# Optimization experiments

Hardware: AMD Instinct MI355X
Metric: run time of the kernel (lower is better)

Reference implementation:

```python
import jax, jax.numpy as jnp
import numpy as np

N, T, D, H = 32, 1024, 1152, 16
DH = D // H            # 72
MLP = int(D * 4.0)     # 4608
EPS = 1e-6


def setup_inputs() -> dict:
    key = jax.random.key(0)
    ks = jax.random.split(key, 14)
    s = 0.02
    return {
        "x": jax.random.normal(ks[0], (N, T, D), jnp.float32),
        "c": jax.random.normal(ks[1], (N, D), jnp.float32),
        "qkv_w": jax.random.normal(ks[2], (D, 3 * D), jnp.float32) * s,
        "qkv_b": jax.random.normal(ks[3], (3 * D,), jnp.float32) * s,
        "proj_w": jax.random.normal(ks[4], (D, D), jnp.float32) * s,
        "proj_b": jax.random.normal(ks[5], (D,), jnp.float32) * s,
        "fc1_w": jax.random.normal(ks[6], (D, MLP), jnp.float32) * s,
        "fc1_b": jax.random.normal(ks[7], (MLP,), jnp.float32) * s,
        "fc2_w": jax.random.normal(ks[8], (MLP, D), jnp.float32) * s,
        "fc2_b": jax.random.normal(ks[9], (D,), jnp.float32) * s,
        "ada_w": jax.random.normal(ks[10], (D, 6 * D), jnp.float32) * s,
        "ada_b": jax.random.normal(ks[11], (6 * D,), jnp.float32) * s,
    }


def _layernorm(x):
    m = jnp.mean(x, axis=-1, keepdims=True)
    v = jnp.var(x, axis=-1, keepdims=True)
    return (x - m) * jax.lax.rsqrt(v + EPS)


def _modulate(x, shift, scale):
    # shift, scale: (N, D) broadcast over T
    return x * (1.0 + scale[:, None, :]) + shift[:, None, :]


def _attention(x, qkv_w, qkv_b, proj_w, proj_b):
    n, t, d = x.shape
    scale = DH ** (-0.5)
    qkv = x @ qkv_w + qkv_b                       # (N,T,3D)
    qkv = qkv.reshape(n, t, 3, H, DH)
    q, k, v = qkv[:, :, 0], qkv[:, :, 1], qkv[:, :, 2]  # each (N,T,H,DH)
    # Faithful to source: matmul over the LAST two dims -> per-token
    # head-vs-head attention of shape (N,T,H,H), softmax over heads.
    attn = jnp.einsum("nthd,ntkd->nthk", q * scale, k)
    attn = jax.nn.softmax(attn, axis=-1)
    out = jnp.einsum("nthk,ntkd->nthd", attn, v)  # (N,T,H,DH)
    out = out.transpose(0, 2, 1, 3).reshape(n, t, d)  # faithful scramble
    return out @ proj_w + proj_b


def _mlp(x, fc1_w, fc1_b, fc2_w, fc2_b):
    h = jax.nn.gelu(x @ fc1_w + fc1_b, approximate=False)  # exact GELU (torch default)
    return h @ fc2_w + fc2_b


def reference(x, c, qkv_w, qkv_b, proj_w, proj_b, fc1_w, fc1_b, fc2_w, fc2_b,
              ada_w, ada_b):
    ada = jax.nn.silu(c) @ ada_w + ada_b          # (N, 6D)
    (shift_msa, scale_msa, gate_msa,
     shift_mlp, scale_mlp, gate_mlp) = jnp.split(ada, 6, axis=1)
    x = x + gate_msa[:, None, :] * _attention(
        _modulate(_layernorm(x), shift_msa, scale_msa),
        qkv_w, qkv_b, proj_w, proj_b)
    x = x + gate_mlp[:, None, :] * _mlp(
        _modulate(_layernorm(x), shift_mlp, scale_mlp),
        fc1_w, fc1_b, fc2_w, fc2_b)
    return x
```

## Files before the change

kernel.cpp:

```cpp
#include <hip/hip_runtime.h>

#define DEV __device__ __forceinline__

typedef __attribute__((ext_vector_type(8))) short short8;
typedef __attribute__((ext_vector_type(8))) __bf16 bf16x8;
typedef __attribute__((ext_vector_type(4))) float f32x4;

#define TD      1024
#define DD      1152
#define DHH     72
#define MLPD    4608
#define QKVN    3456
#define ADAN    6912
#define MROWS   32768

DEV unsigned short f32_to_bf16(float f) {
  unsigned int u = __float_as_uint(f);
  u += 0x7fffu + ((u >> 16) & 1u);
  return (unsigned short)(u >> 16);
}

DEV void gl16(const void* g, void* l) {
  __builtin_amdgcn_global_load_lds((__attribute__((address_space(1))) void*)g,
                                   (__attribute__((address_space(3))) void*)l,
                                   16, 0, 0);
}

DEV bf16x8 zero_bf16x8() {
  short8 z = {0, 0, 0, 0, 0, 0, 0, 0};
  return __builtin_bit_cast(bf16x8, z);
}

DEV float gelu_exact(float v) {
  return 0.5f * v * (1.0f + erff(v * 0.70710678118654752f));
}

#define WAITV(n) asm volatile("s_waitcnt vmcnt(" #n ")" ::: "memory")

__global__ __launch_bounds__(256) void wtrans_kernel(const float* __restrict__ W,
                                                     unsigned short* __restrict__ Wt,
                                                     int K, int N) {
  __shared__ unsigned short tile[32][33];
  const int nb = blockIdx.x * 32, kb = blockIdx.y * 32;
  const int tx = threadIdx.x, ty = threadIdx.y;
  #pragma unroll
  for (int i = ty; i < 32; i += 8)
    tile[i][tx] = f32_to_bf16(W[(size_t)(kb + i) * N + nb + tx]);
  __syncthreads();
  #pragma unroll
  for (int i = ty; i < 32; i += 8)
    Wt[(size_t)(nb + i) * K + kb + tx] = tile[tx][i];
}

__global__ __launch_bounds__(256) void ada_kernel(const float* __restrict__ c,
                                                  const float* __restrict__ ada_w,
                                                  const float* __restrict__ ada_b,
                                                  float* __restrict__ ada_out) {
  __shared__ float sc[DD];
  const int n = blockIdx.y;
  const int col = blockIdx.x * 256 + threadIdx.x;
  for (int i = threadIdx.x; i < DD; i += 256) {
    float v = c[(size_t)n * DD + i];
    sc[i] = v / (1.0f + __expf(-v));
  }
  __syncthreads();
  float acc = ada_b[col];
  #pragma unroll 8
  for (int k = 0; k < DD; ++k)
    acc += sc[k] * ada_w[(size_t)k * ADAN + col];
  ada_out[(size_t)n * ADAN + col] = acc;
}

__global__ __launch_bounds__(256) void ln_mod_kernel(const float* __restrict__ X,
                                                     const float* __restrict__ ada,
                                                     int soff,
                                                     unsigned short* __restrict__ out) {
  const int row = blockIdx.x;
  const int batch = row >> 10;
  const float* xr = X + (size_t)row * DD;
  const int t = threadIdx.x;

  float4 v0 = reinterpret_cast<const float4*>(xr)[t];
  float4 v1 = make_float4(0.f, 0.f, 0.f, 0.f);
  const bool has2 = (t < 32);
  if (has2) v1 = reinterpret_cast<const float4*>(xr)[256 + t];

  float s  = v0.x + v0.y + v0.z + v0.w + v1.x + v1.y + v1.z + v1.w;
  float sq = v0.x*v0.x + v0.y*v0.y + v0.z*v0.z + v0.w*v0.w
           + v1.x*v1.x + v1.y*v1.y + v1.z*v1.z + v1.w*v1.w;
  #pragma unroll
  for (int m = 1; m < 64; m <<= 1) {
    s  += __shfl_xor(s, m);
    sq += __shfl_xor(sq, m);
  }
  __shared__ float red[8];
  const int wv = t >> 6;
  if ((t & 63) == 0) { red[wv] = s; red[4 + wv] = sq; }
  __syncthreads();
  s  = red[0] + red[1] + red[2] + red[3];
  sq = red[4] + red[5] + red[6] + red[7];
  const float mean = s * (1.0f / 1152.0f);
  const float var  = sq * (1.0f / 1152.0f) - mean * mean;
  const float rstd = rsqrtf(var + 1e-6f);

  const float* shp = ada + (size_t)batch * ADAN + soff;
  const float* scp = shp + DD;
  unsigned short* orow = out + (size_t)row * DD;

  {
    const int col = t * 4;
    ushort4 o4;
    o4.x = f32_to_bf16((v0.x - mean) * rstd * (1.0f + scp[col + 0]) + shp[col + 0]);
    o4.y = f32_to_bf16((v0.y - mean) * rstd * (1.0f + scp[col + 1]) + shp[col + 1]);
    o4.z = f32_to_bf16((v0.z - mean) * rstd * (1.0f + scp[col + 2]) + shp[col + 2]);
    o4.w = f32_to_bf16((v0.w - mean) * rstd * (1.0f + scp[col + 3]) + shp[col + 3]);
    reinterpret_cast<ushort4*>(orow)[t] = o4;
  }
  if (has2) {
    const int col = 1024 + t * 4;
    ushort4 o4;
    o4.x = f32_to_bf16((v1.x - mean) * rstd * (1.0f + scp[col + 0]) + shp[col + 0]);
    o4.y = f32_to_bf16((v1.y - mean) * rstd * (1.0f + scp[col + 1]) + shp[col + 1]);
    o4.z = f32_to_bf16((v1.z - mean) * rstd * (1.0f + scp[col + 2]) + shp[col + 2]);
    o4.w = f32_to_bf16((v1.w - mean) * rstd * (1.0f + scp[col + 3]) + shp[col + 3]);
    reinterpret_cast<ushort4*>(orow)[256 + t] = o4;
  }
}

template <int EPI>
__global__ __launch_bounds__(512) void gemm8p(
    const unsigned short* __restrict__ A, const unsigned short* __restrict__ Bt,
    const float* __restrict__ bias, const float* __restrict__ ada, int ada_off,
    const float* __restrict__ resid, unsigned short* __restrict__ out_bf,
    float* __restrict__ out_f, int N, int K, int ntn) {
  __shared__ unsigned short lds[65536];
  const int tid = threadIdx.x;
  const int lane = tid & 63, w = tid >> 6;
  const int wm = w >> 2, wn = w & 3;
  const int l15 = lane & 15, lg = lane >> 4;

  const int nwg = 128 * ntn, cpx = nwg >> 3;
  const int wg = (blockIdx.x & 7) * cpx + (blockIdx.x >> 3);
  const int bm = wg / ntn, bn = wg - bm * ntn;

  const unsigned short* __restrict__ Ag = A + (size_t)bm * 256 * K;
  const unsigned short* __restrict__ Bg = Bt + (size_t)bn * 256 * K;

  const int rp0 = tid >> 3;
  const int ch0 = (tid & 7) ^ (rp0 & 7);

#define STGU(P, RS, LB, BUFB, KT) do {                                                   \
    gl16((P) + (size_t)((RS) + rp0) * K + (size_t)(KT) * 64 + ch0 * 8,                   \
         &lds[(BUFB) + (LB) + tid * 8]);                                                 \
    gl16((P) + (size_t)((RS) + rp0 + 64) * K + (size_t)(KT) * 64 + ch0 * 8,              \
         &lds[(BUFB) + (LB) + 4096 + tid * 8]);                                          \
  } while (0)

  const int chA0 = (lg ^ (l15 & 7)) * 8;
  const int chA1 = chA0 ^ 32;
  const int arow0 = wm * 64 + l15;
  const int brow0 = wn * 32 + l15;

  f32x4 acc[2][2][4][2];
  #pragma unroll
  for (int a = 0; a < 2; ++a)
    #pragma unroll
    for (int b = 0; b < 2; ++b)
      #pragma unroll
      for (int m = 0; m < 4; ++m)
        #pragma unroll
        for (int n2 = 0; n2 < 2; ++n2)
          acc[a][b][m][n2] = (f32x4){0.f, 0.f, 0.f, 0.f};

#define LDA_FROM(PTR, DST, MQ)                                                           \
  _Pragma("unroll") for (int mf = 0; mf < 4; ++mf) {                                     \
    DST[mf][0] = *(const bf16x8*)&(PTR)[(arow0 + (MQ)*128 + mf*16) * 64 + chA0];         \
    DST[mf][1] = *(const bf16x8*)&(PTR)[(arow0 + (MQ)*128 + mf*16) * 64 + chA1];         \
  }
#define LDB_FROM(PTR, DST, NQ)                                                           \
  _Pragma("unroll") for (int nf = 0; nf < 2; ++nf) {                                     \
    DST[nf][0] = *(const bf16x8*)&(PTR)[16384 + (brow0 + (NQ)*128 + nf*16) * 64 + chA0]; \
    DST[nf][1] = *(const bf16x8*)&(PTR)[16384 + (brow0 + (NQ)*128 + nf*16) * 64 + chA1]; \
  }
#define QMFMA(MQ, NQ, AA, BB)                                                            \
  do {                                                                                   \
    __builtin_amdgcn_s_setprio(1);                                                       \
    _Pragma("unroll") for (int mf = 0; mf < 4; ++mf)                                     \
      _Pragma("unroll") for (int nf = 0; nf < 2; ++nf) {                                 \
        acc[MQ][NQ][mf][nf] = __builtin_amdgcn_mfma_f32_16x16x32_bf16(                   \
            AA[mf][0], BB[nf][0], acc[MQ][NQ][mf][nf], 0, 0, 0);                         \
        acc[MQ][NQ][mf][nf] = __builtin_amdgcn_mfma_f32_16x16x32_bf16(                   \
            AA[mf][1], BB[nf][1], acc[MQ][NQ][mf][nf], 0, 0, 0);                         \
      }                                                                                  \
    __builtin_amdgcn_s_setprio(0);                                                       \
  } while (0)

  const int NT = K >> 6;

  STGU(Ag, 0, 0, 0, 0);
  STGU(Bg, 0, 16384, 0, 0);
  STGU(Bg, 128, 24576, 0, 0);
  STGU(Ag, 128, 8192, 0, 0);
  WAITV(4);
  __builtin_amdgcn_s_barrier();

  for (int t = 0; t < NT - 1; ++t) {
    const int cb = (t & 1) << 15, nb = cb ^ 32768;
    const unsigned short* lb = lds + cb;
    bf16x8 a0[4][2], a1[4][2], b0[2][2], b1[2][2];
    LDA_FROM(lb, a0, 0)
    LDB_FROM(lb, b0, 0)
    STGU(Ag, 0, 0, nb, t + 1);
    WAITV(4);
    __builtin_amdgcn_s_barrier();
    QMFMA(0, 0, a0, b0);
    LDB_FROM(lb, b1, 1)
    STGU(Bg, 0, 16384, nb, t + 1);
    WAITV(4);
    __builtin_amdgcn_s_barrier();
    QMFMA(0, 1, a0, b1);
    LDA_FROM(lb, a1, 1)
    STGU(Bg, 128, 24576, nb, t + 1);
    QMFMA(1, 1, a1, b1);
    STGU(Ag, 128, 8192, nb, t + 1);
    WAITV(4);
    __builtin_amdgcn_s_barrier();
    QMFMA(1, 0, a1, b0);
  }
  {
    const int cb = ((NT - 1) & 1) << 15;
    const unsigned short* lb = lds + cb;
    bf16x8 a0[4][2], a1[4][2], b0[2][2], b1[2][2];
    LDA_FROM(lb, a0, 0)
    LDB_FROM(lb, b0, 0)
    WAITV(2);
    __builtin_amdgcn_s_barrier();
    QMFMA(0, 0, a0, b0);
    LDB_FROM(lb, b1, 1)
    WAITV(0);
    __builtin_amdgcn_s_barrier();
    QMFMA(0, 1, a0, b1);
    LDA_FROM(lb, a1, 1)
    QMFMA(1, 1, a1, b1);
    QMFMA(1, 0, a1, b0);
  }
#undef STGU
#undef LDA_FROM
#undef LDB_FROM
#undef QMFMA

  const int batch = bm >> 2;
  #pragma unroll
  for (int nq = 0; nq < 2; ++nq) {
    const int colbase = bn * 256 + nq * 128 + wn * 32;
    if (colbase >= N) continue;
    #pragma unroll
    for (int nf = 0; nf < 2; ++nf) {
      const int colg = colbase + nf * 16 + l15;
      const float bv = bias[colg];
      float g2 = 0.0f;
      if constexpr (EPI == 1 || EPI == 3) g2 = ada[(size_t)batch * ADAN + ada_off + colg];
      #pragma unroll
      for (int mq = 0; mq < 2; ++mq) {
        #pragma unroll
        for (int mf = 0; mf < 4; ++mf) {
          #pragma unroll
          for (int r = 0; r < 4; ++r) {
            const size_t row = (size_t)bm * 256 + wm * 64 + mq * 128 + mf * 16 + lg * 4 + r;
            const size_t idx = row * (size_t)N + colg;
            const float v = acc[mq][nq][mf][nf][r] + bv;
            if constexpr (EPI == 0)      out_bf[idx] = f32_to_bf16(v);
            else if constexpr (EPI == 2) out_bf[idx] = f32_to_bf16(gelu_exact(v));
            else if constexpr (EPI == 1) out_f[idx] = resid[idx] + g2 * v;
            else                         out_f[idx] = out_f[idx] + g2 * v;
          }
        }
      }
    }
  }
}

__global__ __launch_bounds__(256) void attn_kernel(const unsigned short* __restrict__ qkv,
                                                   unsigned short* __restrict__ y) {
  const int tid = threadIdx.x, w = tid >> 6, lane = tid & 63;
  const int l15 = lane & 15, lg = lane >> 4;
  const int tok = blockIdx.x * 4 + w;
  const int n = tok >> 10, t = tok & 1023;

  __shared__ unsigned short Pl[4][16 * 32];
  __shared__ unsigned short Vl[4][16 * 80];

  for (int i = lane; i < 16 * 32; i += 64)
    if ((i & 31) >= 16) Pl[w][i] = 0;

  const size_t rowb = (size_t)tok * QKVN;
  const float scale = 0.11785113019775793f;

  bf16x8 aq[3];
  #pragma unroll
  for (int kk = 0; kk < 3; ++kk) {
    const int d0 = kk * 32 + lg * 8;
    aq[kk] = (d0 < DHH) ? *(const bf16x8*)&qkv[rowb + l15 * DHH + d0] : zero_bf16x8();
  }

  for (int c = lane; c < 144; c += 64) {
    const int r = c / 9, cc = (c % 9) * 8;
    *(short8*)&Vl[w][r * 80 + cc] = *(const short8*)&qkv[rowb + 2 * DD + r * DHH + cc];
  }

  f32x4 s = (f32x4){0.f, 0.f, 0.f, 0.f};
  #pragma unroll
  for (int kk = 0; kk < 3; ++kk) {
    const int d0 = kk * 32 + lg * 8;
    bf16x8 bk = (d0 < DHH) ? *(const bf16x8*)&qkv[rowb + DD + l15 * DHH + d0] : zero_bf16x8();
    s = __builtin_amdgcn_mfma_f32_16x16x32_bf16(aq[kk], bk, s, 0, 0, 0);
  }

  float p[4], mx[4], ssum[4];
  #pragma unroll
  for (int r = 0; r < 4; ++r) { p[r] = s[r] * scale; mx[r] = p[r]; }
  #pragma unroll
  for (int mk = 1; mk <= 8; mk <<= 1)
    #pragma unroll
    for (int r = 0; r < 4; ++r) mx[r] = fmaxf(mx[r], __shfl_xor(mx[r], mk));
  #pragma unroll
  for (int r = 0; r < 4; ++r) { p[r] = __expf(p[r] - mx[r]); ssum[r] = p[r]; }
  #pragma unroll
  for (int mk = 1; mk <= 8; mk <<= 1)
    #pragma unroll
    for (int r = 0; r < 4; ++r) ssum[r] += __shfl_xor(ssum[r], mk);

  #pragma unroll
  for (int r = 0; r < 4; ++r)
    Pl[w][(lg * 4 + r) * 32 + l15] = f32_to_bf16(p[r] / ssum[r]);

  bf16x8 pa = *(const bf16x8*)&Pl[w][l15 * 32 + lg * 8];
  const int kb = (lg & 1) * 8;
  f32x4 o[5];
  #pragma unroll
  for (int df = 0; df < 5; ++df) {
    short8 bvv;
    #pragma unroll
    for (int j = 0; j < 8; ++j)
      bvv[j] = (short)Vl[w][(kb + j) * 80 + df * 16 + l15];
    o[df] = __builtin_amdgcn_mfma_f32_16x16x32_bf16(
        pa, __builtin_bit_cast(bf16x8, bvv), (f32x4){0.f, 0.f, 0.f, 0.f}, 0, 0, 0);
  }

  unsigned short* yb = y + (size_t)n * (TD * DD);
  #pragma unroll
  for (int df = 0; df < 5; ++df) {
    const int d = df * 16 + l15;
    if (d < DHH) {
      #pragma unroll
      for (int r = 0; r < 4; ++r) {
        const int h = lg * 4 + r;
        yb[h * 73728 + t * DHH + d] = f32_to_bf16(o[df][r]);
      }
    }
  }
}

extern "C" void kernel_launch(void* const* d_in, const int* in_sizes, int n_in,
                              void* d_out, int out_size, void* d_ws, size_t ws_size,
                              hipStream_t stream) {
  (void)in_sizes; (void)n_in; (void)out_size; (void)ws_size;
  const float* x      = (const float*)d_in[0];
  const float* c      = (const float*)d_in[1];
  const float* qkv_w  = (const float*)d_in[2];
  const float* qkv_b  = (const float*)d_in[3];
  const float* proj_w = (const float*)d_in[4];
  const float* proj_b = (const float*)d_in[5];
  const float* fc1_w  = (const float*)d_in[6];
  const float* fc1_b  = (const float*)d_in[7];
  const float* fc2_w  = (const float*)d_in[8];
  const float* fc2_b  = (const float*)d_in[9];
  const float* ada_w  = (const float*)d_in[10];
  const float* ada_b  = (const float*)d_in[11];
  float* out = (float*)d_out;

  char* ws = (char*)d_ws;
  unsigned short* hbuf    = (unsigned short*)ws;
  unsigned short* qkvbuf  = hbuf;
  unsigned short* attnbuf = hbuf + (size_t)MROWS * QKVN;
  size_t off = 301989888ull;
  unsigned short* xm    = (unsigned short*)(ws + off); off += 75497472ull;
  unsigned short* wtq   = (unsigned short*)(ws + off); off += (size_t)3584 * DD * 2;
  unsigned short* wtp   = (unsigned short*)(ws + off); off += (size_t)1280 * DD * 2;
  unsigned short* wtf1  = (unsigned short*)(ws + off); off += (size_t)4608 * DD * 2;
  unsigned short* wtf2  = (unsigned short*)(ws + off); off += (size_t)1280 * MLPD * 2;
  float*          adab  = (float*)(ws + off); off += 884736ull;

  const dim3 tb(32, 8);
  hipLaunchKernelGGL(wtrans_kernel, dim3(QKVN / 32, DD / 32), tb, 0, stream, qkv_w, wtq, DD, QKVN);
  hipLaunchKernelGGL(wtrans_kernel, dim3(DD / 32, DD / 32),   tb, 0, stream, proj_w, wtp, DD, DD);
  hipLaunchKernelGGL(wtrans_kernel, dim3(MLPD / 32, DD / 32), tb, 0, stream, fc1_w, wtf1, DD, MLPD);
  hipLaunchKernelGGL(wtrans_kernel, dim3(DD / 32, MLPD / 32), tb, 0, stream, fc2_w, wtf2, MLPD, DD);

  hipLaunchKernelGGL(ada_kernel, dim3(ADAN / 256, 32), dim3(256), 0, stream, c, ada_w, ada_b, adab);

  hipLaunchKernelGGL(ln_mod_kernel, dim3(MROWS), dim3(256), 0, stream, x, adab, 0, xm);

  hipLaunchKernelGGL((gemm8p<0>), dim3(128 * 14), dim3(512), 0, stream,
                     xm, wtq, qkv_b, nullptr, 0, nullptr, qkvbuf, nullptr, QKVN, DD, 14);

  hipLaunchKernelGGL(attn_kernel, dim3(MROWS / 4), dim3(256), 0, stream, qkvbuf, attnbuf);

  hipLaunchKernelGGL((gemm8p<1>), dim3(128 * 5), dim3(512), 0, stream,
                     attnbuf, wtp, proj_b, adab, 2304, x, nullptr, out, DD, DD, 5);

  hipLaunchKernelGGL(ln_mod_kernel, dim3(MROWS), dim3(256), 0, stream, out, adab, 3456, xm);

  hipLaunchKernelGGL((gemm8p<2>), dim3(128 * 18), dim3(512), 0, stream,
                     xm, wtf1, fc1_b, nullptr, 0, nullptr, hbuf, nullptr, MLPD, DD, 18);

  hipLaunchKernelGGL((gemm8p<3>), dim3(128 * 5), dim3(512), 0, stream,
                     hbuf, wtf2, fc2_b, adab, 5760, nullptr, nullptr, out, DD, MLPD, 5);
}
```

Baseline: 1.775 ms.

## Deepen GEMM global-to-LDS prefetch to two tiles ahead with ping-pong barriers

Restructures the GEMM main loop so global-to-LDS loads are issued up to two K-tiles ahead, reusing the current buffer once its fragments are in registers. Adds extra workgroup barriers between MFMA quadrants and merges the epilogue iteration into the loop with guarded loads. The aim is to hide more global memory latency behind MFMA work. The cost is more barriers per iteration and tighter reasoning about buffer reuse hazards.

```diff
diff --git a/kernel.cpp b/kernel.cpp
--- a/kernel.cpp
+++ b/kernel.cpp
@@ -201,48 +201,41 @@
   STGU(Bg, 0, 16384, 0, 0);
   STGU(Bg, 128, 24576, 0, 0);
   STGU(Ag, 128, 8192, 0, 0);
-  WAITV(4);
+  STGU(Ag, 0, 0, 32768, 1);
+  STGU(Bg, 0, 16384, 32768, 1);
+  STGU(Bg, 128, 24576, 32768, 1);
+  WAITV(6);
   __builtin_amdgcn_s_barrier();
 
-  for (int t = 0; t < NT - 1; ++t) {
+  for (int t = 0; t < NT; ++t) {
     const int cb = (t & 1) << 15, nb = cb ^ 32768;
     const unsigned short* lb = lds + cb;
     bf16x8 a0[4][2], a1[4][2], b0[2][2], b1[2][2];
     LDA_FROM(lb, a0, 0)
     LDB_FROM(lb, b0, 0)
-    STGU(Ag, 0, 0, nb, t + 1);
-    WAITV(4);
+    if (t + 1 < NT) STGU(Ag, 128, 8192, nb, t + 1);
     __builtin_amdgcn_s_barrier();
     QMFMA(0, 0, a0, b0);
+    __builtin_amdgcn_s_barrier();
     LDB_FROM(lb, b1, 1)
-    STGU(Bg, 0, 16384, nb, t + 1);
-    WAITV(4);
+    if (t + 2 < NT) STGU(Ag, 0, 0, cb, t + 2);
     __builtin_amdgcn_s_barrier();
     QMFMA(0, 1, a0, b1);
+    __builtin_amdgcn_s_barrier();
     LDA_FROM(lb, a1, 1)
-    STGU(Bg, 128, 24576, nb, t + 1);
+    if (t + 2 < NT) STGU(Bg, 0, 16384, cb, t + 2);
+    __builtin_amdgcn_s_barrier();
     QMFMA(1, 1, a1, b1);
-    STGU(Ag, 128, 8192, nb, t + 1);
-    WAITV(4);
+    __builtin_amdgcn_s_barrier();
+    if (t + 2 < NT) {
+      STGU(Bg, 128, 24576, cb, t + 2);
+      WAITV(6);
+    } else if (t + 1 < NT) {
+      WAITV(0);
+    }
     __builtin_amdgcn_s_barrier();
     QMFMA(1, 0, a1, b0);
-  }
-  {
-    const int cb = ((NT - 1) & 1) << 15;
-    const unsigned short* lb = lds + cb;
-    bf16x8 a0[4][2], a1[4][2], b0[2][2], b1[2][2];
-    LDA_FROM(lb, a0, 0)
-    LDB_FROM(lb, b0, 0)
-    WAITV(2);
-    __builtin_amdgcn_s_barrier();
-    QMFMA(0, 0, a0, b0);
-    LDB_FROM(lb, b1, 1)
-    WAITV(0);
-    __builtin_amdgcn_s_barrier();
-    QMFMA(0, 1, a0, b1);
-    LDA_FROM(lb, a1, 1)
-    QMFMA(1, 1, a1, b1);
-    QMFMA(1, 0, a1, b0);
+    __builtin_amdgcn_s_barrier();
   }
 #undef STGU
 #undef LDA_FROM
```

New measurement: 1.802 ms. No clear change (+1.6%).

## Use 256x128-tile GEMM for QKV and proj to remove N padding waste

Applied to the files above, without the earlier changes.

Adds a new GEMM kernel with a 256x128 output tile, double-buffered LDS staging via direct global-to-LDS loads, and a simple two-stage loop. The QKV and projection GEMMs switch to it, so N tiles divide 3456 and 1152 exactly (27 and 9 tiles) instead of padding to multiples of 256 (3584, 1280). The weight-transpose buffers are shrunk to match. This removes wasted MFMA work on padded columns, but the smaller tile means more A re-reads and possibly less latency hiding than the deeper-pipelined original kernel.

```diff
diff --git a/kernel.cpp b/kernel.cpp
--- a/kernel.cpp
+++ b/kernel.cpp
@@ -280,6 +280,103 @@
   }
 }
 
+template <int EPI>
+__global__ __launch_bounds__(512) void gemm3b(
+    const unsigned short* __restrict__ A, const unsigned short* __restrict__ Bt,
+    const float* __restrict__ bias, const float* __restrict__ ada, int ada_off,
+    const float* __restrict__ resid, unsigned short* __restrict__ out_bf,
+    float* __restrict__ out_f, int N, int K, int ntn) {
+  __shared__ unsigned short lds[24576];
+  const int tid = threadIdx.x;
+  const int lane = tid & 63, w = tid >> 6;
+  const int wm = w >> 1, wn = w & 1;
+  const int l15 = lane & 15, lg = lane >> 4;
+
+  const int nwg = 128 * ntn, cpx = nwg >> 3;
+  const int wg = (blockIdx.x & 7) * cpx + (blockIdx.x >> 3);
+  const int bm = wg / ntn, bn = wg - bm * ntn;
+
+  const unsigned short* __restrict__ Ag = A + (size_t)bm * 256 * K;
+  const unsigned short* __restrict__ Bg = Bt + (size_t)bn * 128 * K;
+
+  const int srow = tid >> 2;
+  const int gch = ((tid & 3) ^ ((tid >> 3) & 3)) * 8;
+
+#define STG(SL, KT) do {                                                                 \
+    gl16(Ag + (size_t)srow * K + (size_t)(KT) * 32 + gch, &lds[(SL) + tid * 8]);         \
+    gl16(Ag + (size_t)(srow + 128) * K + (size_t)(KT) * 32 + gch,                        \
+         &lds[(SL) + 4096 + tid * 8]);                                                   \
+    gl16(Bg + (size_t)srow * K + (size_t)(KT) * 32 + gch,                                \
+         &lds[(SL) + 8192 + tid * 8]);                                                   \
+  } while (0)
+
+  const int chA = (lg ^ ((l15 >> 1) & 3)) * 8;
+  const int arow0 = wm * 64 + l15;
+  const int brow0 = wn * 64 + l15;
+
+  f32x4 acc[4][4];
+  #pragma unroll
+  for (int m = 0; m < 4; ++m)
+    #pragma unroll
+    for (int nn = 0; nn < 4; ++nn)
+      acc[m][nn] = (f32x4){0.f, 0.f, 0.f, 0.f};
+
+  const int NT = K >> 5;
+
+  STG(0, 0);
+  for (int t = 0; t < NT; ++t) {
+    const int sl = (t & 1) * 12288, ns = sl ^ 12288;
+    if (t + 1 < NT) {
+      STG(ns, t + 1);
+      WAITV(3);
+    } else {
+      WAITV(0);
+    }
+    __builtin_amdgcn_s_barrier();
+
+    const unsigned short* lb = lds + sl;
+    bf16x8 af[4], bfv[4];
+    #pragma unroll
+    for (int mf = 0; mf < 4; ++mf)
+      af[mf] = *(const bf16x8*)&lb[(arow0 + mf * 16) * 32 + chA];
+    #pragma unroll
+    for (int nf = 0; nf < 4; ++nf)
+      bfv[nf] = *(const bf16x8*)&lb[8192 + (brow0 + nf * 16) * 32 + chA];
+    __builtin_amdgcn_s_setprio(1);
+    #pragma unroll
+    for (int mf = 0; mf < 4; ++mf)
+      #pragma unroll
+      for (int nf = 0; nf < 4; ++nf)
+        acc[mf][nf] = __builtin_amdgcn_mfma_f32_16x16x32_bf16(af[mf], bfv[nf], acc[mf][nf], 0, 0, 0);
+    __builtin_amdgcn_s_setprio(0);
+    __builtin_amdgcn_s_barrier();
+  }
+#undef STG
+
+  const int batch = bm >> 2;
+  const size_t row0 = (size_t)bm * 256 + wm * 64;
+  const int col0 = bn * 128 + wn * 64;
+  #pragma unroll
+  for (int nf = 0; nf < 4; ++nf) {
+    const int colg = col0 + nf * 16 + l15;
+    const float bv = bias[colg];
+    float g2 = 0.0f;
+    if constexpr (EPI == 1 || EPI == 3) g2 = ada[(size_t)batch * ADAN + ada_off + colg];
+    #pragma unroll
+    for (int mf = 0; mf < 4; ++mf) {
+      #pragma unroll
+      for (int r = 0; r < 4; ++r) {
+        const size_t idx = (row0 + mf * 16 + lg * 4 + r) * (size_t)N + colg;
+        const float v = acc[mf][nf][r] + bv;
+        if constexpr (EPI == 0)      out_bf[idx] = f32_to_bf16(v);
+        else if constexpr (EPI == 2) out_bf[idx] = f32_to_bf16(gelu_exact(v));
+        else if constexpr (EPI == 1) out_f[idx] = resid[idx] + g2 * v;
+        else                         out_f[idx] = out_f[idx] + g2 * v;
+      }
+    }
+  }
+}
+
 __global__ __launch_bounds__(256) void attn_kernel(const unsigned short* __restrict__ qkv,
                                                    unsigned short* __restrict__ y) {
   const int tid = threadIdx.x, w = tid >> 6, lane = tid & 63;
@@ -385,9 +482,9 @@
   unsigned short* attnbuf = hbuf + (size_t)MROWS * QKVN;
   size_t off = 301989888ull;
   unsigned short* xm    = (unsigned short*)(ws + off); off += 75497472ull;
-  unsigned short* wtq   = (unsigned short*)(ws + off); off += (size_t)3584 * DD * 2;
-  unsigned short* wtp   = (unsigned short*)(ws + off); off += (size_t)1280 * DD * 2;
-  unsigned short* wtf1  = (unsigned short*)(ws + off); off += (size_t)4608 * DD * 2;
+  unsigned short* wtq   = (unsigned short*)(ws + off); off += (size_t)QKVN * DD * 2;
+  unsigned short* wtp   = (unsigned short*)(ws + off); off += (size_t)DD * DD * 2;
+  unsigned short* wtf1  = (unsigned short*)(ws + off); off += (size_t)MLPD * DD * 2;
   unsigned short* wtf2  = (unsigned short*)(ws + off); off += (size_t)1280 * MLPD * 2;
   float*          adab  = (float*)(ws + off); off += 884736ull;
 
@@ -401,13 +498,13 @@
 
   hipLaunchKernelGGL(ln_mod_kernel, dim3(MROWS), dim3(256), 0, stream, x, adab, 0, xm);
 
-  hipLaunchKernelGGL((gemm8p<0>), dim3(128 * 14), dim3(512), 0, stream,
-                     xm, wtq, qkv_b, nullptr, 0, nullptr, qkvbuf, nullptr, QKVN, DD, 14);
+  hipLaunchKernelGGL((gemm3b<0>), dim3(128 * 27), dim3(512), 0, stream,
+                     xm, wtq, qkv_b, nullptr, 0, nullptr, qkvbuf, nullptr, QKVN, DD, 27);
 
   hipLaunchKernelGGL(attn_kernel, dim3(MROWS / 4), dim3(256), 0, stream, qkvbuf, attnbuf);
 
-  hipLaunchKernelGGL((gemm8p<1>), dim3(128 * 5), dim3(512), 0, stream,
-                     attnbuf, wtp, proj_b, adab, 2304, x, nullptr, out, DD, DD, 5);
+  hipLaunchKernelGGL((gemm3b<1>), dim3(128 * 9), dim3(512), 0, stream,
+                     attnbuf, wtp, proj_b, adab, 2304, x, nullptr, out, DD, DD, 9);
 
   hipLaunchKernelGGL(ln_mod_kernel, dim3(MROWS), dim3(256), 0, stream, out, adab, 3456, xm);
 
```

After: 1.759 ms (median of 2 runs). About the same (-0.9%).
